# Performance work log

Hardware: AMD Instinct MI355X
Metric: run time of the kernel (lower is better)

## Reference

```python
import jax, jax.numpy as jnp
import numpy as np


def setup_inputs() -> dict:
    key = jax.random.key(0)
    k1, k2 = jax.random.split(key)
    B, Tc, Tq, D = 8, 2048, 1024, 1024
    similarity = jax.random.normal(k1, (B, Tc, Tq), dtype=jnp.float32)
    qencode = jax.random.normal(k2, (B, Tq, D), dtype=jnp.float32)
    return {"similarity": similarity, "qencode": qencode}


def reference(similarity, qencode):
    # softmax over query axis, then weighted sum of query encodings:
    # equivalent to softmax(similarity, -1) @ qencode, avoiding the
    # [B, Tc, Tq, D] broadcasted intermediate of the original TF code.
    attn = jax.nn.softmax(similarity, axis=-1)          # [B, Tc, Tq]
    c2q = jnp.einsum("bcq,bqd->bcd", attn, qencode)     # [B, Tc, D]
    return c2q
```

## Files before the change

kernel.cpp:

```cpp
#include <hip/hip_runtime.h>
#include <hip/hip_bf16.h>
#include <stdint.h>

#define BATCH 8
#define TC 2048
#define TQ 1024
#define DD 1024

typedef __attribute__((ext_vector_type(8))) __bf16 bf16x8;
typedef __attribute__((ext_vector_type(4))) float f32x4;
typedef __attribute__((ext_vector_type(8))) ushort ushort8v;

__device__ __forceinline__ ushort f2bf(float f) {
    uint32_t u = __float_as_uint(f);
    uint32_t r = (u + 0x7fffu + ((u >> 16) & 1u)) >> 16;
    return (ushort)r;
}

__global__ __launch_bounds__(256) void softmax2(const float* __restrict__ sim,
                                                ushort* __restrict__ attn) {
    const int t = threadIdx.x;
    const int wid = t >> 6, lane = t & 63;
    const int r0 = blockIdx.x * 8 + wid * 2;

    const float4* s0 = (const float4*)(sim + (size_t)r0 * TQ);
    const float4* s1 = (const float4*)(sim + (size_t)(r0 + 1) * TQ);

    float4 x0[4], x1[4];
    #pragma unroll
    for (int j = 0; j < 4; j++) { x0[j] = s0[lane + 64 * j]; x1[j] = s1[lane + 64 * j]; }

    float m0 = -INFINITY, m1 = -INFINITY;
    #pragma unroll
    for (int j = 0; j < 4; j++) {
        m0 = fmaxf(m0, fmaxf(fmaxf(x0[j].x, x0[j].y), fmaxf(x0[j].z, x0[j].w)));
        m1 = fmaxf(m1, fmaxf(fmaxf(x1[j].x, x1[j].y), fmaxf(x1[j].z, x1[j].w)));
    }
    #pragma unroll
    for (int o = 32; o >= 1; o >>= 1) {
        m0 = fmaxf(m0, __shfl_xor(m0, o));
        m1 = fmaxf(m1, __shfl_xor(m1, o));
    }

    const float L2E = 1.4426950408889634f;
    float sa = 0.f, sb = 0.f;
    #pragma unroll
    for (int j = 0; j < 4; j++) {
        x0[j].x = exp2f((x0[j].x - m0) * L2E);
        x0[j].y = exp2f((x0[j].y - m0) * L2E);
        x0[j].z = exp2f((x0[j].z - m0) * L2E);
        x0[j].w = exp2f((x0[j].w - m0) * L2E);
        sa += (x0[j].x + x0[j].y) + (x0[j].z + x0[j].w);
        x1[j].x = exp2f((x1[j].x - m1) * L2E);
        x1[j].y = exp2f((x1[j].y - m1) * L2E);
        x1[j].z = exp2f((x1[j].z - m1) * L2E);
        x1[j].w = exp2f((x1[j].w - m1) * L2E);
        sb += (x1[j].x + x1[j].y) + (x1[j].z + x1[j].w);
    }
    #pragma unroll
    for (int o = 32; o >= 1; o >>= 1) {
        sa += __shfl_xor(sa, o);
        sb += __shfl_xor(sb, o);
    }
    const float iva = 1.0f / sa, ivb = 1.0f / sb;

    ushort4* d0 = (ushort4*)(attn + (size_t)r0 * TQ);
    ushort4* d1 = (ushort4*)(attn + (size_t)(r0 + 1) * TQ);
    #pragma unroll
    for (int j = 0; j < 4; j++) {
        ushort4 o4;
        o4.x = f2bf(x0[j].x * iva);
        o4.y = f2bf(x0[j].y * iva);
        o4.z = f2bf(x0[j].z * iva);
        o4.w = f2bf(x0[j].w * iva);
        d0[lane + 64 * j] = o4;
        o4.x = f2bf(x1[j].x * ivb);
        o4.y = f2bf(x1[j].y * ivb);
        o4.z = f2bf(x1[j].z * ivb);
        o4.w = f2bf(x1[j].w * ivb);
        d1[lane + 64 * j] = o4;
    }
}

__global__ __launch_bounds__(256) void transp(const float* __restrict__ qen,
                                              ushort* __restrict__ qt) {
    __shared__ float tile[64][133];
    const int t = threadIdx.x;
    const int bid = blockIdx.x;
    const int b = bid >> 7;
    const int rem = bid & 127;
    const int q0 = (rem >> 3) * 64;
    const int d0 = (rem & 7) * 128;

    const int r0 = t >> 5;
    const int cf = (t & 31) * 4;

    float4 v[8];
    #pragma unroll
    for (int it = 0; it < 8; it++)
        v[it] = *(const float4*)(qen + ((size_t)b * TQ + q0 + r0 + it * 8) * DD + d0 + cf);
    #pragma unroll
    for (int it = 0; it < 8; it++) {
        tile[r0 + it * 8][cf + 0] = v[it].x;
        tile[r0 + it * 8][cf + 1] = v[it].y;
        tile[r0 + it * 8][cf + 2] = v[it].z;
        tile[r0 + it * 8][cf + 3] = v[it].w;
    }
    __syncthreads();

    const int q8 = (t & 7) * 8;
    const int dbase = t >> 3;
    #pragma unroll
    for (int j2 = 0; j2 < 4; j2++) {
        const int d = dbase + 32 * j2;
        ushort8v pk;
        #pragma unroll
        for (int j = 0; j < 8; j++) pk[j] = f2bf(tile[q8 + j][d]);
        *(ushort8v*)(qt + ((size_t)b * DD + d0 + d) * TQ + q0 + q8) = pk;
    }
}

__global__ __launch_bounds__(256, 2) void gemm_bf16(const ushort* __restrict__ A,
                                                    const ushort* __restrict__ Bt,
                                                    float* __restrict__ C) {
    __shared__ __align__(16) ushort As[128 * 64];
    __shared__ __align__(16) ushort Bs[128 * 64];

    const int flat = blockIdx.x;
    const int b = flat & 7;
    const int rem = flat >> 3;
    const int group = rem >> 5;
    const int mi_t = group * 4 + (rem & 3);
    const int ni_t = (rem >> 2) & 7;
    const int tm0 = mi_t * 128;
    const int tn0 = ni_t * 128;

    const ushort* Ab = A + (size_t)b * TC * TQ;
    const ushort* Bb = Bt + (size_t)b * DD * TQ;
    float* Cb = C + (size_t)b * TC * DD;

    const int t = threadIdx.x;
    const int w = t >> 6, lane = t & 63;
    const int quad = lane >> 4, l16 = lane & 15;
    const int wm = (w >> 1) * 64, wn = (w & 1) * 64;

    f32x4 acc[4][4];
    #pragma unroll
    for (int i = 0; i < 4; i++)
        #pragma unroll
        for (int j = 0; j < 4; j++) acc[i][j] = (f32x4){0.f, 0.f, 0.f, 0.f};

    const int srow = w * 8 + (lane >> 3);
    const int sk = ((lane & 7) ^ (lane >> 3)) * 8;

    const int rkey = l16 & 7;

    for (int kk = 0; kk < TQ; kk += 64) {
        #pragma unroll
        for (int i = 0; i < 4; i++) {
            const ushort* ga = Ab + (size_t)(tm0 + i * 32 + srow) * TQ + kk + sk;
            const ushort* gb = Bb + (size_t)(tn0 + i * 32 + srow) * TQ + kk + sk;
            char* la = (char*)As + i * 4096 + w * 1024;
            char* lb = (char*)Bs + i * 4096 + w * 1024;
            __builtin_amdgcn_global_load_lds(
                (const __attribute__((address_space(1))) void*)ga,
                (__attribute__((address_space(3))) void*)la, 16, 0, 0);
            __builtin_amdgcn_global_load_lds(
                (const __attribute__((address_space(1))) void*)gb,
                (__attribute__((address_space(3))) void*)lb, 16, 0, 0);
        }
        __syncthreads();

        #pragma unroll
        for (int s = 0; s < 2; s++) {
            const int rswz = ((s * 4 + quad) ^ rkey) * 8;
            bf16x8 af[4], bfr[4];
            #pragma unroll
            for (int mi = 0; mi < 4; mi++)
                af[mi] = *(const bf16x8*)&As[(wm + mi * 16 + l16) * 64 + rswz];
            #pragma unroll
            for (int ni = 0; ni < 4; ni++)
                bfr[ni] = *(const bf16x8*)&Bs[(wn + ni * 16 + l16) * 64 + rswz];

            #pragma unroll
            for (int mi = 0; mi < 4; mi++)
                #pragma unroll
                for (int ni = 0; ni < 4; ni++)
                    acc[mi][ni] = __builtin_amdgcn_mfma_f32_16x16x32_bf16(
                        af[mi], bfr[ni], acc[mi][ni], 0, 0, 0);
        }
        __syncthreads();
    }

    #pragma unroll
    for (int mi = 0; mi < 4; mi++) {
        const int r0 = tm0 + wm + mi * 16 + quad * 4;
        #pragma unroll
        for (int ni = 0; ni < 4; ni++) {
            const int c = tn0 + wn + ni * 16 + l16;
            f32x4 v = acc[mi][ni];
            #pragma unroll
            for (int r = 0; r < 4; r++) Cb[(size_t)(r0 + r) * DD + c] = v[r];
        }
    }
}

extern "C" void kernel_launch(void* const* d_in, const int* in_sizes, int n_in,
                              void* d_out, int out_size, void* d_ws, size_t ws_size,
                              hipStream_t stream) {
    const float* sim = (const float*)d_in[0];
    const float* qen = (const float*)d_in[1];
    float* out = (float*)d_out;

    ushort* attn = (ushort*)d_ws;
    ushort* qt = (ushort*)d_ws + (size_t)BATCH * TC * TQ;

    softmax2<<<BATCH * TC / 8, 256, 0, stream>>>(sim, attn);
    transp<<<BATCH * (TQ / 64) * (DD / 128), 256, 0, stream>>>(qen, qt);
    gemm_bf16<<<BATCH * (TC / 128) * (DD / 128), 256, 0, stream>>>(attn, qt, out);
}
```

Before: 177.7 us.

## Merge softmax and transpose into one launch, raise GEMM occupancy, nontemporal stores

Folds the softmax kernel and the qencode transpose kernel into a single launch. The first 2048 blocks do the softmax and the rest transpose smaller 64x64 tiles, which removes one kernel launch and lets both phases overlap on the GPU. The GEMM launch bounds go from 2 to 4 blocks per CU to raise occupancy, at the risk of register pressure or spills with its 64 float accumulators per thread. The fp32 output writes become nontemporal stores to reduce cache pollution.

Measured after the change: 178.0 us. About the same (+0.2%).

```diff
diff --git a/kernel.cpp b/kernel.cpp
--- a/kernel.cpp
+++ b/kernel.cpp
@@ -17,110 +17,107 @@
     return (ushort)r;
 }
 
-__global__ __launch_bounds__(256) void softmax2(const float* __restrict__ sim,
-                                                ushort* __restrict__ attn) {
+__global__ __launch_bounds__(256) void prep2(const float* __restrict__ sim,
+                                             const float* __restrict__ qen,
+                                             ushort* __restrict__ attn,
+                                             ushort* __restrict__ qt) {
+    __shared__ float tile[64][65];
     const int t = threadIdx.x;
-    const int wid = t >> 6, lane = t & 63;
-    const int r0 = blockIdx.x * 8 + wid * 2;
-
-    const float4* s0 = (const float4*)(sim + (size_t)r0 * TQ);
-    const float4* s1 = (const float4*)(sim + (size_t)(r0 + 1) * TQ);
-
-    float4 x0[4], x1[4];
-    #pragma unroll
-    for (int j = 0; j < 4; j++) { x0[j] = s0[lane + 64 * j]; x1[j] = s1[lane + 64 * j]; }
-
-    float m0 = -INFINITY, m1 = -INFINITY;
-    #pragma unroll
-    for (int j = 0; j < 4; j++) {
-        m0 = fmaxf(m0, fmaxf(fmaxf(x0[j].x, x0[j].y), fmaxf(x0[j].z, x0[j].w)));
-        m1 = fmaxf(m1, fmaxf(fmaxf(x1[j].x, x1[j].y), fmaxf(x1[j].z, x1[j].w)));
+    if (blockIdx.x < 2048) {
+        const int wid = t >> 6, lane = t & 63;
+        const int r0 = blockIdx.x * 8 + wid * 2;
+
+        const float4* s0 = (const float4*)(sim + (size_t)r0 * TQ);
+        const float4* s1 = (const float4*)(sim + (size_t)(r0 + 1) * TQ);
+
+        float4 x0[4], x1[4];
+        #pragma unroll
+        for (int j = 0; j < 4; j++) { x0[j] = s0[lane + 64 * j]; x1[j] = s1[lane + 64 * j]; }
+
+        float m0 = -INFINITY, m1 = -INFINITY;
+        #pragma unroll
+        for (int j = 0; j < 4; j++) {
+            m0 = fmaxf(m0, fmaxf(fmaxf(x0[j].x, x0[j].y), fmaxf(x0[j].z, x0[j].w)));
+            m1 = fmaxf(m1, fmaxf(fmaxf(x1[j].x, x1[j].y), fmaxf(x1[j].z, x1[j].w)));
+        }
+        #pragma unroll
+        for (int o = 32; o >= 1; o >>= 1) {
+            m0 = fmaxf(m0, __shfl_xor(m0, o));
+            m1 = fmaxf(m1, __shfl_xor(m1, o));
+        }
+
+        const float L2E = 1.4426950408889634f;
+        float sa = 0.f, sb = 0.f;
+        #pragma unroll
+        for (int j = 0; j < 4; j++) {
+            x0[j].x = exp2f((x0[j].x - m0) * L2E);
+            x0[j].y = exp2f((x0[j].y - m0) * L2E);
+            x0[j].z = exp2f((x0[j].z - m0) * L2E);
+            x0[j].w = exp2f((x0[j].w - m0) * L2E);
+            sa += (x0[j].x + x0[j].y) + (x0[j].z + x0[j].w);
+            x1[j].x = exp2f((x1[j].x - m1) * L2E);
+            x1[j].y = exp2f((x1[j].y - m1) * L2E);
+            x1[j].z = exp2f((x1[j].z - m1) * L2E);
+            x1[j].w = exp2f((x1[j].w - m1) * L2E);
+            sb += (x1[j].x + x1[j].y) + (x1[j].z + x1[j].w);
+        }
+        #pragma unroll
+        for (int o = 32; o >= 1; o >>= 1) {
+            sa += __shfl_xor(sa, o);
+            sb += __shfl_xor(sb, o);
+        }
+        const float iva = 1.0f / sa, ivb = 1.0f / sb;
+
+        ushort4* d0 = (ushort4*)(attn + (size_t)r0 * TQ);
+        ushort4* d1 = (ushort4*)(attn + (size_t)(r0 + 1) * TQ);
+        #pragma unroll
+        for (int j = 0; j < 4; j++) {
+            ushort4 o4;
+            o4.x = f2bf(x0[j].x * iva);
+            o4.y = f2bf(x0[j].y * iva);
+            o4.z = f2bf(x0[j].z * iva);
+            o4.w = f2bf(x0[j].w * iva);
+            d0[lane + 64 * j] = o4;
+            o4.x = f2bf(x1[j].x * ivb);
+            o4.y = f2bf(x1[j].y * ivb);
+            o4.z = f2bf(x1[j].z * ivb);
+            o4.w = f2bf(x1[j].w * ivb);
+            d1[lane + 64 * j] = o4;
+        }
+    } else {
+        const int bid = blockIdx.x - 2048;
+        const int b = bid >> 8;
+        const int rem = bid & 255;
+        const int q0 = (rem >> 4) * 64;
+        const int d0 = (rem & 15) * 64;
+        const int r = t >> 4;
+        const int c = (t & 15) * 4;
+
+        #pragma unroll
+        for (int it = 0; it < 4; it++) {
+            float4 v = *(const float4*)(qen + ((size_t)b * TQ + q0 + r + it * 16) * DD + d0 + c);
+            tile[r + it * 16][c + 0] = v.x;
+            tile[r + it * 16][c + 1] = v.y;
+            tile[r + it * 16][c + 2] = v.z;
+            tile[r + it * 16][c + 3] = v.w;
+        }
+        __syncthreads();
+
+        #pragma unroll
+        for (int it = 0; it < 4; it++) {
+            const int d = (t >> 4) + it * 16;
+            const int qq = (t & 15) * 4;
+            ushort4 o4;
+            o4.x = f2bf(tile[qq + 0][d]);
+            o4.y = f2bf(tile[qq + 1][d]);
+            o4.z = f2bf(tile[qq + 2][d]);
+            o4.w = f2bf(tile[qq + 3][d]);
+            *(ushort4*)(qt + ((size_t)b * DD + d0 + d) * TQ + q0 + qq) = o4;
+        }
     }
-    #pragma unroll
-    for (int o = 32; o >= 1; o >>= 1) {
-        m0 = fmaxf(m0, __shfl_xor(m0, o));
-        m1 = fmaxf(m1, __shfl_xor(m1, o));
-    }
-
-    const float L2E = 1.4426950408889634f;
-    float sa = 0.f, sb = 0.f;
-    #pragma unroll
-    for (int j = 0; j < 4; j++) {
-        x0[j].x = exp2f((x0[j].x - m0) * L2E);
-        x0[j].y = exp2f((x0[j].y - m0) * L2E);
-        x0[j].z = exp2f((x0[j].z - m0) * L2E);
-        x0[j].w = exp2f((x0[j].w - m0) * L2E);
-        sa += (x0[j].x + x0[j].y) + (x0[j].z + x0[j].w);
-        x1[j].x = exp2f((x1[j].x - m1) * L2E);
-        x1[j].y = exp2f((x1[j].y - m1) * L2E);
-        x1[j].z = exp2f((x1[j].z - m1) * L2E);
-        x1[j].w = exp2f((x1[j].w - m1) * L2E);
-        sb += (x1[j].x + x1[j].y) + (x1[j].z + x1[j].w);
-    }
-    #pragma unroll
-    for (int o = 32; o >= 1; o >>= 1) {
-        sa += __shfl_xor(sa, o);
-        sb += __shfl_xor(sb, o);
-    }
-    const float iva = 1.0f / sa, ivb = 1.0f / sb;
-
-    ushort4* d0 = (ushort4*)(attn + (size_t)r0 * TQ);
-    ushort4* d1 = (ushort4*)(attn + (size_t)(r0 + 1) * TQ);
-    #pragma unroll
-    for (int j = 0; j < 4; j++) {
-        ushort4 o4;
-        o4.x = f2bf(x0[j].x * iva);
-        o4.y = f2bf(x0[j].y * iva);
-        o4.z = f2bf(x0[j].z * iva);
-        o4.w = f2bf(x0[j].w * iva);
-        d0[lane + 64 * j] = o4;
-        o4.x = f2bf(x1[j].x * ivb);
-        o4.y = f2bf(x1[j].y * ivb);
-        o4.z = f2bf(x1[j].z * ivb);
-        o4.w = f2bf(x1[j].w * ivb);
-        d1[lane + 64 * j] = o4;
-    }
-}
-
-__global__ __launch_bounds__(256) void transp(const float* __restrict__ qen,
-                                              ushort* __restrict__ qt) {
-    __shared__ float tile[64][133];
-    const int t = threadIdx.x;
-    const int bid = blockIdx.x;
-    const int b = bid >> 7;
-    const int rem = bid & 127;
-    const int q0 = (rem >> 3) * 64;
-    const int d0 = (rem & 7) * 128;
-
-    const int r0 = t >> 5;
-    const int cf = (t & 31) * 4;
-
-    float4 v[8];
-    #pragma unroll
-    for (int it = 0; it < 8; it++)
-        v[it] = *(const float4*)(qen + ((size_t)b * TQ + q0 + r0 + it * 8) * DD + d0 + cf);
-    #pragma unroll
-    for (int it = 0; it < 8; it++) {
-        tile[r0 + it * 8][cf + 0] = v[it].x;
-        tile[r0 + it * 8][cf + 1] = v[it].y;
-        tile[r0 + it * 8][cf + 2] = v[it].z;
-        tile[r0 + it * 8][cf + 3] = v[it].w;
-    }
-    __syncthreads();
-
-    const int q8 = (t & 7) * 8;
-    const int dbase = t >> 3;
-    #pragma unroll
-    for (int j2 = 0; j2 < 4; j2++) {
-        const int d = dbase + 32 * j2;
-        ushort8v pk;
-        #pragma unroll
-        for (int j = 0; j < 8; j++) pk[j] = f2bf(tile[q8 + j][d]);
-        *(ushort8v*)(qt + ((size_t)b * DD + d0 + d) * TQ + q0 + q8) = pk;
-    }
-}
-
-__global__ __launch_bounds__(256, 2) void gemm_bf16(const ushort* __restrict__ A,
+}
+
+__global__ __launch_bounds__(256, 4) void gemm_bf16(const ushort* __restrict__ A,
                                                     const ushort* __restrict__ Bt,
                                                     float* __restrict__ C) {
     __shared__ __align__(16) ushort As[128 * 64];
@@ -200,7 +197,8 @@
             const int c = tn0 + wn + ni * 16 + l16;
             f32x4 v = acc[mi][ni];
             #pragma unroll
-            for (int r = 0; r < 4; r++) Cb[(size_t)(r0 + r) * DD + c] = v[r];
+            for (int r = 0; r < 4; r++)
+                __builtin_nontemporal_store(v[r], &Cb[(size_t)(r0 + r) * DD + c]);
         }
     }
 }
@@ -215,7 +213,6 @@
     ushort* attn = (ushort*)d_ws;
     ushort* qt = (ushort*)d_ws + (size_t)BATCH * TC * TQ;
 
-    softmax2<<<BATCH * TC / 8, 256, 0, stream>>>(sim, attn);
-    transp<<<BATCH * (TQ / 64) * (DD / 128), 256, 0, stream>>>(qen, qt);
+    prep2<<<2048 + 2048, 256, 0, stream>>>(sim, qen, attn, qt);
     gemm_bf16<<<BATCH * (TC / 128) * (DD / 128), 256, 0, stream>>>(attn, qt, out);
 }
```
